# Kernel tuning notes

Measured on AMD Instinct MI355X. Metric: run time of the kernel, lower is better.

The kernel has to match this reference:

```python
import jax, jax.numpy as jnp
import numpy as np

H = 8       # num_heads
HD = 32     # transformer_head_dim
LN_EPS = 1e-5


def _layernorm(x, g, b):
    m = jnp.mean(x, axis=-1, keepdims=True)
    v = jnp.mean(jnp.square(x - m), axis=-1, keepdims=True)
    return (x - m) * jax.lax.rsqrt(v + LN_EPS) * g + b


def setup_inputs() -> dict:
    key = jax.random.key(0)
    ks = jax.random.split(key, 8)
    D, DFF = 256, 1024
    B, N = 8, 2048
    s = 0.02  # weight init scale
    return {
        "x": jax.random.normal(ks[0], (B, N, D), jnp.float32),
        "w_qkv": jax.random.normal(ks[1], (3 * H * HD, D), jnp.float32) * s,
        "w_out": jax.random.normal(ks[2], (D, H * HD), jnp.float32) * s,
        "b_out": jnp.zeros((D,), jnp.float32),
        "w1": jax.random.normal(ks[3], (DFF, D), jnp.float32) * s,
        "wv": jax.random.normal(ks[4], (DFF, D), jnp.float32) * s,
        "w2": jax.random.normal(ks[5], (D, DFF), jnp.float32) * s,
        "ln1_g": jnp.ones((D,), jnp.float32),
        "ln1_b": jnp.zeros((D,), jnp.float32),
        "ln2_g": jnp.ones((D,), jnp.float32),
        "ln2_b": jnp.zeros((D,), jnp.float32),
    }


def reference(x, w_qkv, w_out, b_out, w1, wv, w2, ln1_g, ln1_b, ln2_g, ln2_b):
    B, N, D = x.shape
    scale = HD ** (-0.5)
    # --- MultiHeadedAttention ---
    qkv = x @ w_qkv.T                                   # [B,N,3*H*HD]
    q, k, v = jnp.split(qkv, 3, axis=-1)
    def to_heads(t):
        return t.reshape(B, N, H, HD).transpose(0, 2, 1, 3)  # [B,H,N,HD]
    q, k, v = to_heads(q), to_heads(k), to_heads(v)
    sim = jnp.einsum("bhid,bhjd->bhij", q, k) * scale   # [B,H,N,N]
    attn = jax.nn.softmax(sim, axis=-1)
    o = jnp.einsum("bhij,bhjd->bhid", attn, v)
    o = o.transpose(0, 2, 1, 3).reshape(B, N, H * HD)
    y = o @ w_out.T + b_out                             # attn output
    # --- attn AddNorm: ln(dropout(y)+x), dropout off ---
    x1 = _layernorm(y + x, ln1_g, ln1_b)
    # --- GEGLU FFN applied to y (faithful to source) ---
    ff = jax.nn.gelu(y @ w1.T, approximate=False) * (y @ wv.T)
    ff = ff @ w2.T
    # --- ff AddNorm ---
    return _layernorm(ff + x1, ln2_g, ln2_b)
```

## Files before the change

kernel.cpp:

```cpp
#include <hip/hip_runtime.h>

typedef unsigned short u16;
typedef __bf16 bf16;
typedef __bf16 bf16x8 __attribute__((ext_vector_type(8)));
typedef __bf16 bf16x4 __attribute__((ext_vector_type(4)));
typedef short s16x4 __attribute__((ext_vector_type(4)));
typedef float f32x4 __attribute__((ext_vector_type(4)));
typedef unsigned short u16x8 __attribute__((ext_vector_type(8)));
typedef unsigned short u16x4 __attribute__((ext_vector_type(4)));
typedef unsigned short u16x2 __attribute__((ext_vector_type(2)));

#define DEVI static __device__ __forceinline__

DEVI float bf2f(u16 h) { return __builtin_bit_cast(float, (unsigned)h << 16); }
DEVI u16 cvt_bf(float f) { return __builtin_bit_cast(u16, (bf16)f); }

DEVI void gload16(const u16* g, u16* l) {
  __builtin_amdgcn_global_load_lds(
      (const __attribute__((address_space(1))) void*)g,
      (__attribute__((address_space(3))) void*)l, 16, 0, 0);
}

DEVI float gelu_exact(float x) {
  return 0.5f * x * (1.0f + erff(x * 0.70710678118654752f));
}

DEVI f32x4 mfma16(bf16x4 a, bf16x4 b, f32x4 c) {
#if __has_builtin(__builtin_amdgcn_mfma_f32_16x16x16bf16_1k)
  return __builtin_amdgcn_mfma_f32_16x16x16bf16_1k(
      __builtin_bit_cast(s16x4, a), __builtin_bit_cast(s16x4, b), c, 0, 0, 0);
#else
  f32x4 r = c;
  asm volatile("s_nop 1\n\tv_mfma_f32_16x16x16_bf16 %0, %1, %2, %0\n\ts_nop 7\n\ts_nop 3"
               : "+v"(r) : "v"(a), "v"(b));
  return r;
#endif
}

__global__ __launch_bounds__(256) void k_cast(const float* __restrict__ x,
                                              const float* __restrict__ wqkv,
                                              const float* __restrict__ wout,
                                              const float* __restrict__ w1,
                                              const float* __restrict__ wv,
                                              const float* __restrict__ w2,
                                              u16* __restrict__ dst0) {
  long i = (long)blockIdx.x * 256 + threadIdx.x;
  const float* src;
  u16* dst;
  long off;
  if (i < 1048576)       { src = x;    dst = dst0;           off = i; }
  else if (i < 1097728)  { src = wqkv; dst = dst0 + 4194304; off = i - 1048576; }
  else if (i < 1114112)  { src = wout; dst = dst0 + 4390912; off = i - 1097728; }
  else if (i < 1179648)  { src = w1;   dst = dst0 + 4456448; off = i - 1114112; }
  else if (i < 1245184)  { src = wv;   dst = dst0 + 4718592; off = i - 1179648; }
  else                   { src = w2;   dst = dst0 + 4980736; off = i - 1245184; }
  float4 f = reinterpret_cast<const float4*>(src)[off];
  u16x4 o;
  o[0] = cvt_bf(f.x); o[1] = cvt_bf(f.y); o[2] = cvt_bf(f.z); o[3] = cvt_bf(f.w);
  reinterpret_cast<u16x4*>(dst)[off] = o;
}

template <int BM, int BN, int NI>
__global__ __launch_bounds__(256) void k_gemm(const u16* __restrict__ A, const u16* __restrict__ B0,
                                              const u16* __restrict__ B1, int Nsplit,
                                              const float* __restrict__ bias,
                                              u16* __restrict__ C, int N, int K) {
  constexpr int MI = BM / 32;
  __shared__ u16 Alds[BM * 64];
  __shared__ u16 Blds[BN * 64];
  const int m0 = blockIdx.x * BM;
  const int n0 = blockIdx.y * BN;
  const u16* Ap = A + (long)m0 * K;
  const u16* Bp = (n0 < Nsplit) ? (B0 + (long)n0 * K) : (B1 + (long)(n0 - Nsplit) * K);
  const int tid = threadIdx.x, lane = tid & 63, wave = tid >> 6;
  const int wr = (wave >> 1) * (BM / 2), wc = (wave & 1) * (BN / 2);
  const int lr = lane & 15, g = lane >> 4;
  const int sr = lane >> 3, sg = lane & 7;

  f32x4 acc[MI][NI] = {};
  const int nk = K >> 6;
  for (int kt = 0; kt < nk; ++kt) {
    const int kb = kt << 6;
    __syncthreads();
#pragma unroll
    for (int c = 0; c < BM / 32; ++c) {
      const int row = wave * (BM / 4) + c * 8 + sr;
      gload16(Ap + (long)row * K + kb + ((sg ^ (row & 7)) << 3),
              &Alds[(wave * (BM / 4) + c * 8) << 6]);
    }
#pragma unroll
    for (int c = 0; c < BN / 32; ++c) {
      const int row = wave * (BN / 4) + c * 8 + sr;
      gload16(Bp + (long)row * K + kb + ((sg ^ ((row / NI) & 7)) << 3),
              &Blds[(wave * (BN / 4) + c * 8) << 6]);
    }
    __syncthreads();
#pragma unroll
    for (int kk = 0; kk < 2; ++kk) {
      bf16x8 av[MI], bv[NI];
#pragma unroll
      for (int i = 0; i < MI; ++i) {
        const int ra = wr + i * 16 + lr;
        av[i] = *reinterpret_cast<const bf16x8*>(&Alds[(ra << 6) + (((kk * 4 + g) ^ (ra & 7)) << 3)]);
      }
#pragma unroll
      for (int ni = 0; ni < NI; ++ni) {
        const int rb = wc + lr * NI + ni;
        bv[ni] = *reinterpret_cast<const bf16x8*>(&Blds[(rb << 6) + (((kk * 4 + g) ^ ((rb / NI) & 7)) << 3)]);
      }
#pragma unroll
      for (int mi = 0; mi < MI; ++mi)
#pragma unroll
        for (int ni = 0; ni < NI; ++ni)
          acc[mi][ni] = __builtin_amdgcn_mfma_f32_16x16x32_bf16(av[mi], bv[ni], acc[mi][ni], 0, 0, 0);
    }
  }
  const int colb = n0 + wc + lr * NI;
  float bvv[NI];
#pragma unroll
  for (int ni = 0; ni < NI; ++ni) bvv[ni] = bias ? bias[colb + ni] : 0.0f;
#pragma unroll
  for (int mi = 0; mi < MI; ++mi) {
#pragma unroll
    for (int r = 0; r < 4; ++r) {
      const long row = m0 + wr + mi * 16 + g * 4 + r;
      if constexpr (NI == 4) {
        u16x4 v;
#pragma unroll
        for (int ni = 0; ni < 4; ++ni) v[ni] = cvt_bf(acc[mi][ni][r] + bvv[ni]);
        *reinterpret_cast<u16x4*>(C + row * N + colb) = v;
      } else {
        u16x2 v;
#pragma unroll
        for (int ni = 0; ni < 2; ++ni) v[ni] = cvt_bf(acc[mi][ni][r] + bvv[ni]);
        *reinterpret_cast<u16x2*>(C + row * N + colb) = v;
      }
    }
  }
}

__global__ __launch_bounds__(256) void k_glu(const u16* __restrict__ A, const u16* __restrict__ W1,
                                             const u16* __restrict__ Wv, u16* __restrict__ C) {
  constexpr int K = 256, N = 1024;
  __shared__ u16 Alds[128 * 64];
  __shared__ u16 Blds[64 * 64];
  const int m0 = blockIdx.x * 128;
  const int n0h = blockIdx.y * 32;
  const u16* Ap = A + (long)m0 * K;
  const int tid = threadIdx.x, lane = tid & 63, wave = tid >> 6;
  const int lr = lane & 15, g = lane >> 4;
  const int sr = lane >> 3, sg = lane & 7;

  f32x4 acc[2][4] = {};
  for (int kt = 0; kt < 4; ++kt) {
    const int kb = kt << 6;
    __syncthreads();
#pragma unroll
    for (int c = 0; c < 4; ++c) {
      const int row = wave * 32 + c * 8 + sr;
      gload16(Ap + (long)row * K + kb + ((sg ^ (row & 7)) << 3), &Alds[(wave * 32 + c * 8) << 6]);
    }
#pragma unroll
    for (int c = 0; c < 2; ++c) {
      const int row = wave * 16 + c * 8 + sr;
      const u16* bp = (row & 1) ? Wv : W1;
      gload16(bp + (long)(n0h + (row >> 1)) * K + kb + ((sg ^ ((row >> 2) & 7)) << 3),
              &Blds[(wave * 16 + c * 8) << 6]);
    }
    __syncthreads();
#pragma unroll
    for (int kk = 0; kk < 2; ++kk) {
      bf16x8 av[2], bv[4];
#pragma unroll
      for (int i = 0; i < 2; ++i) {
        const int ra = wave * 32 + i * 16 + lr;
        av[i] = *reinterpret_cast<const bf16x8*>(&Alds[(ra << 6) + (((kk * 4 + g) ^ (ra & 7)) << 3)]);
      }
#pragma unroll
      for (int ni = 0; ni < 4; ++ni) {
        const int rb = lr * 4 + ni;
        bv[ni] = *reinterpret_cast<const bf16x8*>(&Blds[(rb << 6) + (((kk * 4 + g) ^ ((rb >> 2) & 7)) << 3)]);
      }
#pragma unroll
      for (int mi = 0; mi < 2; ++mi)
#pragma unroll
        for (int ni = 0; ni < 4; ++ni)
          acc[mi][ni] = __builtin_amdgcn_mfma_f32_16x16x32_bf16(av[mi], bv[ni], acc[mi][ni], 0, 0, 0);
    }
  }
  const int j0 = n0h + lr * 2;
#pragma unroll
  for (int mi = 0; mi < 2; ++mi) {
#pragma unroll
    for (int r = 0; r < 4; ++r) {
      const long row = m0 + wave * 32 + mi * 16 + g * 4 + r;
      u16x2 v;
      v[0] = cvt_bf(gelu_exact(acc[mi][0][r]) * acc[mi][1][r]);
      v[1] = cvt_bf(gelu_exact(acc[mi][2][r]) * acc[mi][3][r]);
      *reinterpret_cast<u16x2*>(C + row * N + j0) = v;
    }
  }
}

__global__ __launch_bounds__(256) void k_vt(const u16* __restrict__ qkv, u16* __restrict__ vt) {
  const int bh = blockIdx.x & 63, nt = blockIdx.x >> 6;
  const int b = bh >> 3, h = bh & 7;
  const int wave = threadIdx.x >> 6, lane = threadIdx.x & 63;
  const int dcol = wave * 8;
#pragma unroll
  for (int i = 0; i < 4; ++i) {
    const int nn = nt * 256 + i * 64 + lane;
    u16x8 v = *reinterpret_cast<const u16x8*>(qkv + (long)(b * 2048 + nn) * 768 + 512 + h * 32 + dcol);
#pragma unroll
    for (int j = 0; j < 8; ++j)
      vt[(long)(bh * 32 + dcol + j) * 2048 + nn] = v[j];
  }
}

__global__ __launch_bounds__(512) void k_attn(const u16* __restrict__ qkv, const u16* __restrict__ vt,
                                              u16* __restrict__ o) {
  __shared__ u16 Klds[2 * 4096];
  __shared__ u16 Vlds[2 * 4096];
  const int id = blockIdx.x;
  const int qt = id >> 6, bh = id & 63;
  const int b = bh >> 3, h = bh & 7;
  const int tid = threadIdx.x, wave = tid >> 6, lane = tid & 63;
  const int lq = lane & 15, g = lane >> 4, lqh = lq & 7;

  const long qrow = (long)(b * 2048 + qt * 128 + wave * 16 + lq);
  u16x8 qraw = *reinterpret_cast<const u16x8*>(qkv + qrow * 768 + h * 32 + g * 8);
  bf16x8 qf;
#pragma unroll
  for (int j = 0; j < 8; ++j) qf[j] = (bf16)(bf2f(qraw[j]) * 0.25503486f);

  const int rK = tid >> 3, gpK = tid & 7, lK = gpK ^ (rK & 7);
  const u16* ksrc = qkv + (long)(b * 2048 + (lK >> 2) * 64 + rK) * 768 + 256 + h * 32 + (lK & 3) * 8;
  const int dV = tid >> 4, gpV = tid & 15, lgV = gpV ^ ((dV & 3) << 1);
  const u16* vsrc = vt + (long)(bh * 32 + dV) * 2048 + lgV * 8;
  u16* kdst = Klds + wave * 512;
  u16* vdst = Vlds + wave * 512;

  gload16(ksrc, kdst);
  gload16(vsrc, vdst);

  float m = -1e30f;
  f32x4 oacc[2] = {};
  f32x4 lacc = {};
  const f32x4 zero = {0.0f, 0.0f, 0.0f, 0.0f};
  bf16x4 onesf;
  onesf[0] = onesf[1] = onesf[2] = onesf[3] = (bf16)1.0f;

  for (int kt = 0; kt < 16; ++kt) {
    const int bo = (kt & 1) * 4096;
    __syncthreads();
    if (kt + 1 < 16) {
      const int nbo = ((kt + 1) & 1) * 4096;
      gload16(ksrc + (long)(kt + 1) * 98304, kdst + nbo);
      gload16(vsrc + (kt + 1) * 128, vdst + nbo);
    }
    f32x4 s[8];
#pragma unroll
    for (int f = 0; f < 8; ++f) {
      const bf16x8 kf = *reinterpret_cast<const bf16x8*>(
          &Klds[bo + (((f & 3) * 16 + lq) << 6) + ((((f >> 2) * 4 + g) ^ lqh) << 3)]);
      s[f] = __builtin_amdgcn_mfma_f32_16x16x32_bf16(kf, qf, zero, 0, 0, 0);
    }
    float tmax = -1e30f;
#pragma unroll
    for (int f = 0; f < 8; ++f) {
      const float m01 = fmaxf(s[f][0], s[f][1]);
      const float m23 = fmaxf(s[f][2], s[f][3]);
      tmax = fmaxf(tmax, fmaxf(m01, m23));
    }
    if (__any(tmax > m + 8.0f)) {
      tmax = fmaxf(tmax, __shfl_xor(tmax, 16));
      tmax = fmaxf(tmax, __shfl_xor(tmax, 32));
      const float mnew = fmaxf(m, tmax);
      const float alpha = exp2f(m - mnew);
#pragma unroll
      for (int di = 0; di < 2; ++di)
#pragma unroll
        for (int r = 0; r < 4; ++r) oacc[di][r] *= alpha;
#pragma unroll
      for (int r = 0; r < 4; ++r) lacc[r] *= alpha;
      m = mnew;
    }
#pragma unroll
    for (int f = 0; f < 8; ++f)
#pragma unroll
      for (int r = 0; r < 4; ++r) s[f][r] = exp2f(s[f][r] - m);

#pragma unroll
    for (int f = 0; f < 8; ++f) {
      bf16x4 pf4;
      pf4[0] = (bf16)s[f][0]; pf4[1] = (bf16)s[f][1];
      pf4[2] = (bf16)s[f][2]; pf4[3] = (bf16)s[f][3];
      lacc = mfma16(onesf, pf4, lacc);
      const int gl8 = (f >> 2) * 16 + (f & 3) * 4 + g;
      const int ph8 = gl8 ^ ((lq & 3) << 2);
#pragma unroll
      for (int di = 0; di < 2; ++di) {
        const int d = di * 16 + lq;
        const bf16x4 vf = *reinterpret_cast<const bf16x4*>(&Vlds[bo + d * 128 + ph8 * 4]);
        oacc[di] = mfma16(vf, pf4, oacc[di]);
      }
    }
  }

  const float inv = 1.0f / lacc[0];
  const long orow = (long)(b * 2048 + qt * 128 + wave * 16 + lq);
#pragma unroll
  for (int di = 0; di < 2; ++di) {
    u16x4 ov;
#pragma unroll
    for (int r = 0; r < 4; ++r) ov[r] = cvt_bf(oacc[di][r] * inv);
    *reinterpret_cast<u16x4*>(o + orow * 256 + h * 32 + di * 16 + g * 4) = ov;
  }
}

__global__ __launch_bounds__(256) void k_ln(const u16* __restrict__ yin, const float* __restrict__ xres,
                                            const float* __restrict__ gw, const float* __restrict__ bw,
                                            float* __restrict__ out) {
  const int row = blockIdx.x * 4 + (threadIdx.x >> 6);
  const int lane = threadIdx.x & 63;
  const long base = (long)row * 256 + lane * 4;
  const float4 xv = *reinterpret_cast<const float4*>(xres + base);
  const u16x4 yv = *reinterpret_cast<const u16x4*>(yin + base);
  float s0 = bf2f(yv[0]) + xv.x;
  float s1 = bf2f(yv[1]) + xv.y;
  float s2 = bf2f(yv[2]) + xv.z;
  float s3 = bf2f(yv[3]) + xv.w;
  float sum = s0 + s1 + s2 + s3;
  float sq = s0 * s0 + s1 * s1 + s2 * s2 + s3 * s3;
#pragma unroll
  for (int msk = 1; msk < 64; msk <<= 1) {
    sum += __shfl_xor(sum, msk);
    sq += __shfl_xor(sq, msk);
  }
  const float mean = sum * (1.0f / 256.0f);
  const float var = sq * (1.0f / 256.0f) - mean * mean;
  const float rstd = rsqrtf(var + 1e-5f);
  const int c = lane * 4;
  float4 ov;
  ov.x = (s0 - mean) * rstd * gw[c + 0] + bw[c + 0];
  ov.y = (s1 - mean) * rstd * gw[c + 1] + bw[c + 1];
  ov.z = (s2 - mean) * rstd * gw[c + 2] + bw[c + 2];
  ov.w = (s3 - mean) * rstd * gw[c + 3] + bw[c + 3];
  *reinterpret_cast<float4*>(out + base) = ov;
}

extern "C" void kernel_launch(void* const* d_in, const int* in_sizes, int n_in,
                              void* d_out, int out_size, void* d_ws, size_t ws_size,
                              hipStream_t stream) {
  (void)in_sizes; (void)n_in; (void)out_size;
  if (ws_size < 136314880ULL) return;

  const float* x     = (const float*)d_in[0];
  const float* w_qkv = (const float*)d_in[1];
  const float* w_out = (const float*)d_in[2];
  const float* b_out = (const float*)d_in[3];
  const float* w1    = (const float*)d_in[4];
  const float* wv    = (const float*)d_in[5];
  const float* w2    = (const float*)d_in[6];
  const float* ln1g  = (const float*)d_in[7];
  const float* ln1b  = (const float*)d_in[8];
  const float* ln2g  = (const float*)d_in[9];
  const float* ln2b  = (const float*)d_in[10];
  float* outp = (float*)d_out;

  char* ws = (char*)d_ws;
  u16* xb    = (u16*)ws;
  u16* wqkvb = xb + 4194304;
  u16* woutb = wqkvb + 196608;
  u16* w1b   = woutb + 65536;
  u16* wvb   = w1b + 262144;
  u16* w2b   = wvb + 262144;
  u16* qkvb  = w2b + 262144;
  u16* ob    = qkvb + 12582912;
  u16* yb    = ob + 4194304;
  float* x1  = (float*)(ws + 52428800);
  u16* vtb   = (u16*)(ws + 69206016);
  u16* ffin  = qkvb;
  u16* ff2   = xb;

  k_cast<<<5120, 256, 0, stream>>>(x, w_qkv, w_out, w1, wv, w2, xb);
  k_gemm<128, 128, 4><<<dim3(128, 6), 256, 0, stream>>>(xb, wqkvb, wqkvb, 1 << 30, nullptr, qkvb, 768, 256);
  k_vt<<<512, 256, 0, stream>>>(qkvb, vtb);
  k_attn<<<1024, 512, 0, stream>>>(qkvb, vtb, ob);
  k_gemm<128, 64, 2><<<dim3(128, 4), 256, 0, stream>>>(ob, woutb, woutb, 1 << 30, b_out, yb, 256, 256);
  k_ln<<<4096, 256, 0, stream>>>(yb, x, ln1g, ln1b, x1);
  k_glu<<<dim3(128, 32), 256, 0, stream>>>(yb, w1b, wvb, ffin);
  k_gemm<128, 64, 2><<<dim3(128, 4), 256, 0, stream>>>(ffin, w2b, w2b, 1 << 30, nullptr, ff2, 256, 1024);
  k_ln<<<4096, 256, 0, stream>>>(ff2, x1, ln2g, ln2b, outp);
}
```

Baseline: 276.5 us.

## Double-buffer GEMM LDS tiles and process two query tiles per attention wave

The GEMM and GEGLU kernels gain double-buffered LDS so the next K tile is loaded while the current one is computed, which removes one barrier per iteration. The attention kernel now gives each wave 32 query rows instead of 16, reusing every K and V fragment read from LDS for two MFMA streams, and halves the grid. It also raises wave priority around the MFMA sections. The costs are more registers and LDS per block, possibly lower occupancy, and fewer attention blocks. Whether qt/b/h indexing derived from blockIdx still matches the halved grid depends on lines not shown.

```diff
diff --git a/kernel.cpp b/kernel.cpp
--- a/kernel.cpp
+++ b/kernel.cpp
@@ -66,8 +66,9 @@
                                               const float* __restrict__ bias,
                                               u16* __restrict__ C, int N, int K) {
   constexpr int MI = BM / 32;
-  __shared__ u16 Alds[BM * 64];
-  __shared__ u16 Blds[BN * 64];
+  constexpr int ASZ = BM * 64, BSZ = BN * 64;
+  __shared__ u16 Alds[2 * ASZ];
+  __shared__ u16 Blds[2 * BSZ];
   const int m0 = blockIdx.x * BM;
   const int n0 = blockIdx.y * BN;
   const u16* Ap = A + (long)m0 * K;
@@ -77,36 +78,41 @@
   const int lr = lane & 15, g = lane >> 4;
   const int sr = lane >> 3, sg = lane & 7;
 
-  f32x4 acc[MI][NI] = {};
-  const int nk = K >> 6;
-  for (int kt = 0; kt < nk; ++kt) {
+  auto stage = [&](int kt, int buf) {
     const int kb = kt << 6;
-    __syncthreads();
 #pragma unroll
     for (int c = 0; c < BM / 32; ++c) {
       const int row = wave * (BM / 4) + c * 8 + sr;
       gload16(Ap + (long)row * K + kb + ((sg ^ (row & 7)) << 3),
-              &Alds[(wave * (BM / 4) + c * 8) << 6]);
+              &Alds[buf * ASZ + ((wave * (BM / 4) + c * 8) << 6)]);
     }
 #pragma unroll
     for (int c = 0; c < BN / 32; ++c) {
       const int row = wave * (BN / 4) + c * 8 + sr;
       gload16(Bp + (long)row * K + kb + ((sg ^ ((row / NI) & 7)) << 3),
-              &Blds[(wave * (BN / 4) + c * 8) << 6]);
-    }
+              &Blds[buf * BSZ + ((wave * (BN / 4) + c * 8) << 6)]);
+    }
+  };
+
+  f32x4 acc[MI][NI] = {};
+  const int nk = K >> 6;
+  stage(0, 0);
+  for (int kt = 0; kt < nk; ++kt) {
+    const int ab = (kt & 1) * ASZ, bb = (kt & 1) * BSZ;
     __syncthreads();
+    if (kt + 1 < nk) stage(kt + 1, (kt + 1) & 1);
 #pragma unroll
     for (int kk = 0; kk < 2; ++kk) {
       bf16x8 av[MI], bv[NI];
 #pragma unroll
       for (int i = 0; i < MI; ++i) {
         const int ra = wr + i * 16 + lr;
-        av[i] = *reinterpret_cast<const bf16x8*>(&Alds[(ra << 6) + (((kk * 4 + g) ^ (ra & 7)) << 3)]);
+        av[i] = *reinterpret_cast<const bf16x8*>(&Alds[ab + (ra << 6) + (((kk * 4 + g) ^ (ra & 7)) << 3)]);
       }
 #pragma unroll
       for (int ni = 0; ni < NI; ++ni) {
         const int rb = wc + lr * NI + ni;
-        bv[ni] = *reinterpret_cast<const bf16x8*>(&Blds[(rb << 6) + (((kk * 4 + g) ^ ((rb / NI) & 7)) << 3)]);
+        bv[ni] = *reinterpret_cast<const bf16x8*>(&Blds[bb + (rb << 6) + (((kk * 4 + g) ^ ((rb / NI) & 7)) << 3)]);
       }
 #pragma unroll
       for (int mi = 0; mi < MI; ++mi)
@@ -142,8 +148,9 @@
 __global__ __launch_bounds__(256) void k_glu(const u16* __restrict__ A, const u16* __restrict__ W1,
                                              const u16* __restrict__ Wv, u16* __restrict__ C) {
   constexpr int K = 256, N = 1024;
-  __shared__ u16 Alds[128 * 64];
-  __shared__ u16 Blds[64 * 64];
+  constexpr int ASZ = 128 * 64, BSZ = 64 * 64;
+  __shared__ u16 Alds[2 * ASZ];
+  __shared__ u16 Blds[2 * BSZ];
   const int m0 = blockIdx.x * 128;
   const int n0h = blockIdx.y * 32;
   const u16* Ap = A + (long)m0 * K;
@@ -151,35 +158,41 @@
   const int lr = lane & 15, g = lane >> 4;
   const int sr = lane >> 3, sg = lane & 7;
 
-  f32x4 acc[2][4] = {};
-  for (int kt = 0; kt < 4; ++kt) {
+  auto stage = [&](int kt, int buf) {
     const int kb = kt << 6;
-    __syncthreads();
 #pragma unroll
     for (int c = 0; c < 4; ++c) {
       const int row = wave * 32 + c * 8 + sr;
-      gload16(Ap + (long)row * K + kb + ((sg ^ (row & 7)) << 3), &Alds[(wave * 32 + c * 8) << 6]);
+      gload16(Ap + (long)row * K + kb + ((sg ^ (row & 7)) << 3),
+              &Alds[buf * ASZ + ((wave * 32 + c * 8) << 6)]);
     }
 #pragma unroll
     for (int c = 0; c < 2; ++c) {
       const int row = wave * 16 + c * 8 + sr;
       const u16* bp = (row & 1) ? Wv : W1;
       gload16(bp + (long)(n0h + (row >> 1)) * K + kb + ((sg ^ ((row >> 2) & 7)) << 3),
-              &Blds[(wave * 16 + c * 8) << 6]);
-    }
+              &Blds[buf * BSZ + ((wave * 16 + c * 8) << 6)]);
+    }
+  };
+
+  f32x4 acc[2][4] = {};
+  stage(0, 0);
+  for (int kt = 0; kt < 4; ++kt) {
+    const int ab = (kt & 1) * ASZ, bb = (kt & 1) * BSZ;
     __syncthreads();
+    if (kt + 1 < 4) stage(kt + 1, (kt + 1) & 1);
 #pragma unroll
     for (int kk = 0; kk < 2; ++kk) {
       bf16x8 av[2], bv[4];
 #pragma unroll
       for (int i = 0; i < 2; ++i) {
         const int ra = wave * 32 + i * 16 + lr;
-        av[i] = *reinterpret_cast<const bf16x8*>(&Alds[(ra << 6) + (((kk * 4 + g) ^ (ra & 7)) << 3)]);
+        av[i] = *reinterpret_cast<const bf16x8*>(&Alds[ab + (ra << 6) + (((kk * 4 + g) ^ (ra & 7)) << 3)]);
       }
 #pragma unroll
       for (int ni = 0; ni < 4; ++ni) {
         const int rb = lr * 4 + ni;
-        bv[ni] = *reinterpret_cast<const bf16x8*>(&Blds[(rb << 6) + (((kk * 4 + g) ^ ((rb >> 2) & 7)) << 3)]);
+        bv[ni] = *reinterpret_cast<const bf16x8*>(&Blds[bb + (rb << 6) + (((kk * 4 + g) ^ ((rb >> 2) & 7)) << 3)]);
       }
 #pragma unroll
       for (int mi = 0; mi < 2; ++mi)
@@ -227,11 +240,14 @@
   const int tid = threadIdx.x, wave = tid >> 6, lane = tid & 63;
   const int lq = lane & 15, g = lane >> 4, lqh = lq & 7;
 
-  const long qrow = (long)(b * 2048 + qt * 128 + wave * 16 + lq);
-  u16x8 qraw = *reinterpret_cast<const u16x8*>(qkv + qrow * 768 + h * 32 + g * 8);
-  bf16x8 qf;
-#pragma unroll
-  for (int j = 0; j < 8; ++j) qf[j] = (bf16)(bf2f(qraw[j]) * 0.25503486f);
+  bf16x8 qf[2];
+#pragma unroll
+  for (int qi = 0; qi < 2; ++qi) {
+    const long qrow = (long)(b * 2048 + qt * 256 + wave * 32 + qi * 16 + lq);
+    const u16x8 qraw = *reinterpret_cast<const u16x8*>(qkv + qrow * 768 + h * 32 + g * 8);
+#pragma unroll
+    for (int j = 0; j < 8; ++j) qf[qi][j] = (bf16)(bf2f(qraw[j]) * 0.25503486f);
+  }
 
   const int rK = tid >> 3, gpK = tid & 7, lK = gpK ^ (rK & 7);
   const u16* ksrc = qkv + (long)(b * 2048 + (lK >> 2) * 64 + rK) * 768 + 256 + h * 32 + (lK & 3) * 8;
@@ -243,9 +259,9 @@
   gload16(ksrc, kdst);
   gload16(vsrc, vdst);
 
-  float m = -1e30f;
-  f32x4 oacc[2] = {};
-  f32x4 lacc = {};
+  float m[2] = {-1e30f, -1e30f};
+  f32x4 oacc[2][2] = {};
+  f32x4 lacc[2] = {};
   const f32x4 zero = {0.0f, 0.0f, 0.0f, 0.0f};
   bf16x4 onesf;
   onesf[0] = onesf[1] = onesf[2] = onesf[3] = (bf16)1.0f;
@@ -258,63 +274,76 @@
       gload16(ksrc + (long)(kt + 1) * 98304, kdst + nbo);
       gload16(vsrc + (kt + 1) * 128, vdst + nbo);
     }
-    f32x4 s[8];
+    f32x4 s[2][8];
+    __builtin_amdgcn_s_setprio(1);
 #pragma unroll
     for (int f = 0; f < 8; ++f) {
       const bf16x8 kf = *reinterpret_cast<const bf16x8*>(
           &Klds[bo + (((f & 3) * 16 + lq) << 6) + ((((f >> 2) * 4 + g) ^ lqh) << 3)]);
-      s[f] = __builtin_amdgcn_mfma_f32_16x16x32_bf16(kf, qf, zero, 0, 0, 0);
-    }
-    float tmax = -1e30f;
+      s[0][f] = __builtin_amdgcn_mfma_f32_16x16x32_bf16(kf, qf[0], zero, 0, 0, 0);
+      s[1][f] = __builtin_amdgcn_mfma_f32_16x16x32_bf16(kf, qf[1], zero, 0, 0, 0);
+    }
+    __builtin_amdgcn_s_setprio(0);
+#pragma unroll
+    for (int qi = 0; qi < 2; ++qi) {
+      float tmax = -1e30f;
+#pragma unroll
+      for (int f = 0; f < 8; ++f) {
+        const float m01 = fmaxf(s[qi][f][0], s[qi][f][1]);
+        const float m23 = fmaxf(s[qi][f][2], s[qi][f][3]);
+        tmax = fmaxf(tmax, fmaxf(m01, m23));
+      }
+      if (__any(tmax > m[qi] + 8.0f)) {
+        tmax = fmaxf(tmax, __shfl_xor(tmax, 16));
+        tmax = fmaxf(tmax, __shfl_xor(tmax, 32));
+        const float mnew = fmaxf(m[qi], tmax);
+        const float alpha = exp2f(m[qi] - mnew);
+#pragma unroll
+        for (int di = 0; di < 2; ++di)
+#pragma unroll
+          for (int r = 0; r < 4; ++r) oacc[qi][di][r] *= alpha;
+#pragma unroll
+        for (int r = 0; r < 4; ++r) lacc[qi][r] *= alpha;
+        m[qi] = mnew;
+      }
+#pragma unroll
+      for (int f = 0; f < 8; ++f)
+#pragma unroll
+        for (int r = 0; r < 4; ++r) s[qi][f][r] = exp2f(s[qi][f][r] - m[qi]);
+    }
+    __builtin_amdgcn_s_setprio(1);
 #pragma unroll
     for (int f = 0; f < 8; ++f) {
-      const float m01 = fmaxf(s[f][0], s[f][1]);
-      const float m23 = fmaxf(s[f][2], s[f][3]);
-      tmax = fmaxf(tmax, fmaxf(m01, m23));
-    }
-    if (__any(tmax > m + 8.0f)) {
-      tmax = fmaxf(tmax, __shfl_xor(tmax, 16));
-      tmax = fmaxf(tmax, __shfl_xor(tmax, 32));
-      const float mnew = fmaxf(m, tmax);
-      const float alpha = exp2f(m - mnew);
-#pragma unroll
-      for (int di = 0; di < 2; ++di)
-#pragma unroll
-        for (int r = 0; r < 4; ++r) oacc[di][r] *= alpha;
-#pragma unroll
-      for (int r = 0; r < 4; ++r) lacc[r] *= alpha;
-      m = mnew;
-    }
-#pragma unroll
-    for (int f = 0; f < 8; ++f)
-#pragma unroll
-      for (int r = 0; r < 4; ++r) s[f][r] = exp2f(s[f][r] - m);
-
-#pragma unroll
-    for (int f = 0; f < 8; ++f) {
-      bf16x4 pf4;
-      pf4[0] = (bf16)s[f][0]; pf4[1] = (bf16)s[f][1];
-      pf4[2] = (bf16)s[f][2]; pf4[3] = (bf16)s[f][3];
-      lacc = mfma16(onesf, pf4, lacc);
       const int gl8 = (f >> 2) * 16 + (f & 3) * 4 + g;
       const int ph8 = gl8 ^ ((lq & 3) << 2);
-#pragma unroll
-      for (int di = 0; di < 2; ++di) {
-        const int d = di * 16 + lq;
-        const bf16x4 vf = *reinterpret_cast<const bf16x4*>(&Vlds[bo + d * 128 + ph8 * 4]);
-        oacc[di] = mfma16(vf, pf4, oacc[di]);
-      }
-    }
-  }
-
-  const float inv = 1.0f / lacc[0];
-  const long orow = (long)(b * 2048 + qt * 128 + wave * 16 + lq);
-#pragma unroll
-  for (int di = 0; di < 2; ++di) {
-    u16x4 ov;
-#pragma unroll
-    for (int r = 0; r < 4; ++r) ov[r] = cvt_bf(oacc[di][r] * inv);
-    *reinterpret_cast<u16x4*>(o + orow * 256 + h * 32 + di * 16 + g * 4) = ov;
+      bf16x4 vf[2];
+#pragma unroll
+      for (int di = 0; di < 2; ++di)
+        vf[di] = *reinterpret_cast<const bf16x4*>(&Vlds[bo + (di * 16 + lq) * 128 + ph8 * 4]);
+#pragma unroll
+      for (int qi = 0; qi < 2; ++qi) {
+        bf16x4 pf4;
+        pf4[0] = (bf16)s[qi][f][0]; pf4[1] = (bf16)s[qi][f][1];
+        pf4[2] = (bf16)s[qi][f][2]; pf4[3] = (bf16)s[qi][f][3];
+        lacc[qi] = mfma16(onesf, pf4, lacc[qi]);
+        oacc[qi][0] = mfma16(vf[0], pf4, oacc[qi][0]);
+        oacc[qi][1] = mfma16(vf[1], pf4, oacc[qi][1]);
+      }
+    }
+    __builtin_amdgcn_s_setprio(0);
+  }
+
+#pragma unroll
+  for (int qi = 0; qi < 2; ++qi) {
+    const float inv = 1.0f / lacc[qi][0];
+    const long orow = (long)(b * 2048 + qt * 256 + wave * 32 + qi * 16 + lq);
+#pragma unroll
+    for (int di = 0; di < 2; ++di) {
+      u16x4 ov;
+#pragma unroll
+      for (int r = 0; r < 4; ++r) ov[r] = cvt_bf(oacc[qi][di][r] * inv);
+      *reinterpret_cast<u16x4*>(o + orow * 256 + h * 32 + di * 16 + g * 4) = ov;
+    }
   }
 }
 
@@ -386,7 +415,7 @@
   k_cast<<<5120, 256, 0, stream>>>(x, w_qkv, w_out, w1, wv, w2, xb);
   k_gemm<128, 128, 4><<<dim3(128, 6), 256, 0, stream>>>(xb, wqkvb, wqkvb, 1 << 30, nullptr, qkvb, 768, 256);
   k_vt<<<512, 256, 0, stream>>>(qkvb, vtb);
-  k_attn<<<1024, 512, 0, stream>>>(qkvb, vtb, ob);
+  k_attn<<<512, 512, 0, stream>>>(qkvb, vtb, ob);
   k_gemm<128, 64, 2><<<dim3(128, 4), 256, 0, stream>>>(ob, woutb, woutb, 1 << 30, b_out, yb, 256, 256);
   k_ln<<<4096, 256, 0, stream>>>(yb, x, ln1g, ln1b, x1);
   k_glu<<<dim3(128, 32), 256, 0, stream>>>(yb, w1b, wvb, ffin);
```

New measurement: 286.9 us. +3.8%, slower.
